# Performance work log

Measured on AMD Instinct MI355X. Metric: run time of the kernel, lower is better.

The kernel has to match this reference:

```python
import jax, jax.numpy as jnp
import numpy as np

DECAY = 0.95

def setup_inputs() -> dict:
    key = jax.random.key(0)
    k1, k2, k3, k4 = jax.random.split(key, 4)
    B, S, H, Dk, Dv = 4, 4096, 16, 64, 64
    return {
        "memory": jax.random.normal(k1, (H, Dk, Dv), dtype=jnp.float32),
        "keys": jax.random.normal(k2, (B, S, H, Dk), dtype=jnp.float32),
        "values": jax.random.normal(k3, (B, S, H, Dv), dtype=jnp.float32),
        "write_strengths": jax.random.uniform(k4, (B, S), dtype=jnp.float32),
    }

def reference(memory, keys, values, write_strengths):
    # M_new = decay * M + sum_{b,s} rho[b,s] * k[b,s,h] v[b,s,h]^T
    # Algebraically equivalent to per-head (rho-weighted) K^T V contraction;
    # avoids materializing the (B,S,H,Dk,Dv) outer-product tensor.
    delta = jnp.einsum('bs,bshk,bshv->hkv', write_strengths, keys, values)
    return DECAY * memory + delta
```

## Files before the change

### kernel.cpp

```cpp
#include <hip/hip_runtime.h>
#include <stdint.h>


typedef __bf16  bf16x8  __attribute__((ext_vector_type(8)));
typedef __bf16  bf16x4  __attribute__((ext_vector_type(4)));
typedef short   s16x4   __attribute__((ext_vector_type(4)));
typedef float   floatx4 __attribute__((ext_vector_type(4)));

constexpr int HH   = 16;
constexpr int DK   = 64;
constexpr int DV   = 64;
constexpr int ROWS = 16384;
constexpr int NSLICE = 64;
constexpr int RPB  = ROWS / NSLICE;
constexpr int TR   = 32;
constexpr int NR   = RPB / TR;
constexpr float DECAY = 0.95f;

__global__ __launch_bounds__(256) void init_out(const float* __restrict__ mem,
                                                float* __restrict__ out) {
    int i = blockIdx.x * 256 + threadIdx.x;
    out[i] = DECAY * mem[i];
}

__device__ __forceinline__ unsigned lds_off(const void* p) {
    return (unsigned)(uintptr_t)(__attribute__((address_space(3))) const void*)p;
}

__global__ __launch_bounds__(256, 4) void accum(const float* __restrict__ keys,
                                                const float* __restrict__ values,
                                                const float* __restrict__ rho,
                                                float* __restrict__ out) {
    __shared__ __align__(128) __bf16 kb[2][TR * DK];
    __shared__ __align__(128) __bf16 vb[2][TR * DV];
    __shared__ float rs[RPB];

    const int t    = threadIdx.x;
    const int lane = t & 63;
    const int w    = t >> 6;
    const int wr   = w >> 1;
    const int wc   = w & 1;
    const int m    = lane & 15;
    const int q    = lane >> 4;
    const int h    = blockIdx.y;
    const int row0 = blockIdx.x * RPB;

    rs[t] = rho[row0 + t];

    const int sl0 = t >> 4;
    const int c0  = (t & 15) * 4;

    float4 pk[2], pv[2];

    auto loadr = [&](int r) {
        #pragma unroll
        for (int i = 0; i < 2; ++i) {
            const int sl = sl0 + i * 16;
            const size_t off = ((size_t)(row0 + r * TR + sl) * HH + h) * DK + c0;
            pk[i] = *(const float4*)(keys + off);
            pv[i] = *(const float4*)(values + off);
        }
    };
    auto writer = [&](int r, int b) {
        #pragma unroll
        for (int i = 0; i < 2; ++i) {
            const int sl = sl0 + i * 16;
            const float rv = rs[r * TR + sl];
            bf16x4 kh = {(__bf16)(pk[i].x * rv), (__bf16)(pk[i].y * rv),
                         (__bf16)(pk[i].z * rv), (__bf16)(pk[i].w * rv)};
            bf16x4 vh = {(__bf16)pv[i].x, (__bf16)pv[i].y,
                         (__bf16)pv[i].z, (__bf16)pv[i].w};
            const int eo = ((sl >> 2) * 4 + (c0 >> 4)) * 64 + (sl & 3) * 16 + (c0 & 15);
            *(bf16x4*)&kb[b][eo] = kh;
            *(bf16x4*)&vb[b][eo] = vh;
        }
    };

    floatx4 acc[2][2];
    #pragma unroll
    for (int i = 0; i < 2; ++i)
        #pragma unroll
        for (int j = 0; j < 2; ++j)
            acc[i][j] = (floatx4){0.f, 0.f, 0.f, 0.f};

    loadr(0);
    __syncthreads();
    writer(0, 0);

    for (int r = 0; r < NR; ++r) {
        const int cur = r & 1;
        if (r + 1 < NR) loadr(r + 1);
        __syncthreads();

        const unsigned abase = lds_off(&kb[cur][0]) + q * 1024 + 8 * m;
        const unsigned bbase = lds_off(&vb[cur][0]) + q * 1024 + 8 * m;

        s16x4 alo[2], ahi[2], blo[2], bhi[2];
        #pragma unroll
        for (int mt = 0; mt < 2; ++mt) {
            const unsigned ad = abase + (unsigned)((wr * 2 + mt) * 128);
            asm volatile("ds_read_b64_tr_b16 %0, %1" : "=v"(alo[mt]) : "v"(ad));
            asm volatile("ds_read_b64_tr_b16 %0, %1 offset:512" : "=v"(ahi[mt]) : "v"(ad));
        }
        #pragma unroll
        for (int nt = 0; nt < 2; ++nt) {
            const unsigned bd = bbase + (unsigned)((wc * 2 + nt) * 128);
            asm volatile("ds_read_b64_tr_b16 %0, %1" : "=v"(blo[nt]) : "v"(bd));
            asm volatile("ds_read_b64_tr_b16 %0, %1 offset:512" : "=v"(bhi[nt]) : "v"(bd));
        }
        asm volatile("s_waitcnt lgkmcnt(0)" ::: "memory");
        __builtin_amdgcn_sched_barrier(0);

        bf16x8 af[2], bfv[2];
        #pragma unroll
        for (int mt = 0; mt < 2; ++mt) {
            union { s16x4 hh[2]; bf16x8 v; } u;
            u.hh[0] = alo[mt]; u.hh[1] = ahi[mt];
            af[mt] = u.v;
        }
        #pragma unroll
        for (int nt = 0; nt < 2; ++nt) {
            union { s16x4 hh[2]; bf16x8 v; } u;
            u.hh[0] = blo[nt]; u.hh[1] = bhi[nt];
            bfv[nt] = u.v;
        }

        #pragma unroll
        for (int mt = 0; mt < 2; ++mt)
            #pragma unroll
            for (int nt = 0; nt < 2; ++nt)
                acc[mt][nt] = __builtin_amdgcn_mfma_f32_16x16x32_bf16(
                    af[mt], bfv[nt], acc[mt][nt], 0, 0, 0);

        if (r + 1 < NR) writer(r + 1, cur ^ 1);
    }

    float* o = out + h * (DK * DV) + (wr * 32) * DV + wc * 32;
    #pragma unroll
    for (int mt = 0; mt < 2; ++mt)
        #pragma unroll
        for (int nt = 0; nt < 2; ++nt)
            #pragma unroll
            for (int g = 0; g < 4; ++g)
                atomicAdd(o + (mt * 16 + q * 4 + g) * DV + nt * 16 + m,
                          acc[mt][nt][g]);
}

extern "C" void kernel_launch(void* const* d_in, const int* in_sizes, int n_in,
                              void* d_out, int out_size, void* d_ws, size_t ws_size,
                              hipStream_t stream) {
    const float* mem    = (const float*)d_in[0];
    const float* keys   = (const float*)d_in[1];
    const float* values = (const float*)d_in[2];
    const float* rho    = (const float*)d_in[3];
    float* out = (float*)d_out;

    init_out<<<dim3((HH * DK * DV) / 256), dim3(256), 0, stream>>>(mem, out);

    dim3 grid(NSLICE, HH);
    accum<<<grid, dim3(256), 0, stream>>>(keys, values, rho, out);
}
```

Baseline: 158.1 us.

## Prefetch two tiles ahead and replace atomic reduction with workspace two-stage reduce

The global-load prefetch is deepened from one to two tiles using two register sets, and the next tile's loads are issued after the LDS reads so their latency overlaps the MFMA work. The final cross-slice reduction no longer uses fp32 atomics into the output. When enough workspace is available, each block writes its partial 64x64 tile to the workspace and a separate vectorized kernel sums the 64 slices and applies the decay. This removes atomic contention and the init kernel, at the cost of extra workspace traffic (about 16 MB written and read) and more registers.

```diff
diff --git a/kernel.cpp b/kernel.cpp
--- a/kernel.cpp
+++ b/kernel.cpp
@@ -16,6 +16,7 @@
 constexpr int TR   = 32;
 constexpr int NR   = RPB / TR;
 constexpr float DECAY = 0.95f;
+constexpr size_t WS_NEED = (size_t)NSLICE * HH * DK * DV * sizeof(float);
 
 __global__ __launch_bounds__(256) void init_out(const float* __restrict__ mem,
                                                 float* __restrict__ out) {
@@ -27,10 +28,11 @@
     return (unsigned)(uintptr_t)(__attribute__((address_space(3))) const void*)p;
 }
 
+template <bool TWOSTAGE>
 __global__ __launch_bounds__(256, 4) void accum(const float* __restrict__ keys,
                                                 const float* __restrict__ values,
                                                 const float* __restrict__ rho,
-                                                float* __restrict__ out) {
+                                                float* __restrict__ dst) {
     __shared__ __align__(128) __bf16 kb[2][TR * DK];
     __shared__ __align__(128) __bf16 vb[2][TR * DV];
     __shared__ float rs[RPB];
@@ -50,26 +52,26 @@
     const int sl0 = t >> 4;
     const int c0  = (t & 15) * 4;
 
-    float4 pk[2], pv[2];
-
-    auto loadr = [&](int r) {
+    float4 pk[2][2], pv[2][2];
+
+    auto loadr = [&](int r, int set) {
         #pragma unroll
         for (int i = 0; i < 2; ++i) {
             const int sl = sl0 + i * 16;
             const size_t off = ((size_t)(row0 + r * TR + sl) * HH + h) * DK + c0;
-            pk[i] = *(const float4*)(keys + off);
-            pv[i] = *(const float4*)(values + off);
+            pk[set][i] = *(const float4*)(keys + off);
+            pv[set][i] = *(const float4*)(values + off);
         }
     };
-    auto writer = [&](int r, int b) {
+    auto writer = [&](int r, int set, int b) {
         #pragma unroll
         for (int i = 0; i < 2; ++i) {
             const int sl = sl0 + i * 16;
             const float rv = rs[r * TR + sl];
-            bf16x4 kh = {(__bf16)(pk[i].x * rv), (__bf16)(pk[i].y * rv),
-                         (__bf16)(pk[i].z * rv), (__bf16)(pk[i].w * rv)};
-            bf16x4 vh = {(__bf16)pv[i].x, (__bf16)pv[i].y,
-                         (__bf16)pv[i].z, (__bf16)pv[i].w};
+            bf16x4 kh = {(__bf16)(pk[set][i].x * rv), (__bf16)(pk[set][i].y * rv),
+                         (__bf16)(pk[set][i].z * rv), (__bf16)(pk[set][i].w * rv)};
+            bf16x4 vh = {(__bf16)pv[set][i].x, (__bf16)pv[set][i].y,
+                         (__bf16)pv[set][i].z, (__bf16)pv[set][i].w};
             const int eo = ((sl >> 2) * 4 + (c0 >> 4)) * 64 + (sl & 3) * 16 + (c0 & 15);
             *(bf16x4*)&kb[b][eo] = kh;
             *(bf16x4*)&vb[b][eo] = vh;
@@ -83,13 +85,13 @@
         for (int j = 0; j < 2; ++j)
             acc[i][j] = (floatx4){0.f, 0.f, 0.f, 0.f};
 
-    loadr(0);
+    loadr(0, 0);
+    loadr(1, 1);
     __syncthreads();
-    writer(0, 0);
+    writer(0, 0, 0);
 
     for (int r = 0; r < NR; ++r) {
         const int cur = r & 1;
-        if (r + 1 < NR) loadr(r + 1);
         __syncthreads();
 
         const unsigned abase = lds_off(&kb[cur][0]) + q * 1024 + 8 * m;
@@ -108,6 +110,9 @@
             asm volatile("ds_read_b64_tr_b16 %0, %1" : "=v"(blo[nt]) : "v"(bd));
             asm volatile("ds_read_b64_tr_b16 %0, %1 offset:512" : "=v"(bhi[nt]) : "v"(bd));
         }
+
+        if (r + 2 < NR) loadr(r + 2, cur);
+
         asm volatile("s_waitcnt lgkmcnt(0)" ::: "memory");
         __builtin_amdgcn_sched_barrier(0);
 
@@ -132,18 +137,46 @@
                 acc[mt][nt] = __builtin_amdgcn_mfma_f32_16x16x32_bf16(
                     af[mt], bfv[nt], acc[mt][nt], 0, 0, 0);
 
-        if (r + 1 < NR) writer(r + 1, cur ^ 1);
-    }
-
-    float* o = out + h * (DK * DV) + (wr * 32) * DV + wc * 32;
-    #pragma unroll
-    for (int mt = 0; mt < 2; ++mt)
-        #pragma unroll
-        for (int nt = 0; nt < 2; ++nt)
+        if (r + 1 < NR) writer(r + 1, (r + 1) & 1, (r + 1) & 1);
+    }
+
+    if (TWOSTAGE) {
+        float* o = dst + ((size_t)(blockIdx.x * HH + h)) * (DK * DV)
+                       + (wr * 32) * DV + wc * 32;
+        #pragma unroll
+        for (int mt = 0; mt < 2; ++mt)
             #pragma unroll
-            for (int g = 0; g < 4; ++g)
-                atomicAdd(o + (mt * 16 + q * 4 + g) * DV + nt * 16 + m,
-                          acc[mt][nt][g]);
+            for (int nt = 0; nt < 2; ++nt)
+                #pragma unroll
+                for (int g = 0; g < 4; ++g)
+                    o[(mt * 16 + q * 4 + g) * DV + nt * 16 + m] = acc[mt][nt][g];
+    } else {
+        float* o = dst + h * (DK * DV) + (wr * 32) * DV + wc * 32;
+        #pragma unroll
+        for (int mt = 0; mt < 2; ++mt)
+            #pragma unroll
+            for (int nt = 0; nt < 2; ++nt)
+                #pragma unroll
+                for (int g = 0; g < 4; ++g)
+                    atomicAdd(o + (mt * 16 + q * 4 + g) * DV + nt * 16 + m,
+                              acc[mt][nt][g]);
+    }
+}
+
+__global__ __launch_bounds__(256) void reduce_ws(const float* __restrict__ mem,
+                                                 const float* __restrict__ ws,
+                                                 float* __restrict__ out) {
+    const int i4 = blockIdx.x * 256 + threadIdx.x;
+    const floatx4* wv = (const floatx4*)ws;
+    constexpr int SLAB = HH * DK * DV / 4;
+    floatx4 s0 = {0.f, 0.f, 0.f, 0.f}, s1 = {0.f, 0.f, 0.f, 0.f};
+    #pragma unroll 8
+    for (int sl = 0; sl < NSLICE; sl += 2) {
+        s0 += wv[(size_t)sl * SLAB + i4];
+        s1 += wv[(size_t)(sl + 1) * SLAB + i4];
+    }
+    const floatx4 m4 = ((const floatx4*)mem)[i4];
+    ((floatx4*)out)[i4] = DECAY * m4 + (s0 + s1);
 }
 
 extern "C" void kernel_launch(void* const* d_in, const int* in_sizes, int n_in,
@@ -155,8 +188,13 @@
     const float* rho    = (const float*)d_in[3];
     float* out = (float*)d_out;
 
-    init_out<<<dim3((HH * DK * DV) / 256), dim3(256), 0, stream>>>(mem, out);
-
     dim3 grid(NSLICE, HH);
-    accum<<<grid, dim3(256), 0, stream>>>(keys, values, rho, out);
-}
+    if (ws_size >= WS_NEED) {
+        accum<true><<<grid, dim3(256), 0, stream>>>(keys, values, rho, (float*)d_ws);
+        reduce_ws<<<dim3(HH * DK * DV / 4 / 256), dim3(256), 0, stream>>>(
+            mem, (const float*)d_ws, out);
+    } else {
+        init_out<<<dim3((HH * DK * DV) / 256), dim3(256), 0, stream>>>(mem, out);
+        accum<false><<<grid, dim3(256), 0, stream>>>(keys, values, rho, out);
+    }
+}
```

New measurement: 163.0 us. 3.1% more time.
